# Kernel optimization log

Measured on AMD Instinct MI355X. Metric: run time of the kernel, lower is better.

The kernel has to match this reference:

```python
import jax, jax.numpy as jnp
import numpy as np


def setup_inputs() -> dict:
    key = jax.random.key(0)
    ks = jax.random.split(key, 12)
    C_IN, C = 512, 256  # input_feat_dim, input_feat_dim // 2
    B, H, W = 8, 14, 14
    s = 0.02
    return {
        "im": jax.random.normal(ks[0], (B, C_IN, H, W), dtype=jnp.float32),
        "boxes": jax.random.normal(ks[1], (B, 4, 4), dtype=jnp.float32),
        "normalized_boxes": jax.random.normal(ks[2], (B, 4, 4), dtype=jnp.float32),
        # proj: Conv2d(512, 256, kernel_size=1) -> equivalent to [out, in] matmul
        "proj_w": jax.random.normal(ks[3], (C, C_IN), dtype=jnp.float32) * s,
        "proj_b": jax.random.normal(ks[4], (C,), dtype=jnp.float32) * s,
        # g_mlp: Linear(512,256), Linear(256,256), Linear(256,256); stored [in, out]
        "w1": jax.random.normal(ks[5], (2 * C, C), dtype=jnp.float32) * s,
        "b1": jax.random.normal(ks[6], (C,), dtype=jnp.float32) * s,
        "w2": jax.random.normal(ks[7], (C, C), dtype=jnp.float32) * s,
        "b2": jax.random.normal(ks[8], (C,), dtype=jnp.float32) * s,
        "w3": jax.random.normal(ks[9], (C, C), dtype=jnp.float32) * s,
        "b3": jax.random.normal(ks[10], (C,), dtype=jnp.float32) * s,
    }


def reference(im, boxes, normalized_boxes, proj_w, proj_b, w1, b1, w2, b2, w3, b3):
    # boxes / normalized_boxes are deleted by the original forward.
    del boxes, normalized_boxes
    # 1x1 conv projection: [b, c_in, h, w] -> [b, c, h, w]
    x = jnp.einsum("bihw,oi->bohw", im, proj_w) + proj_b[None, :, None, None]
    b, c, h, w = x.shape
    hw = h * w
    xf = x.reshape(b, c, hw).transpose(0, 2, 1)  # [b, hw, c]
    # Pairwise concat semantics of the original:
    #   x_full[b, k, l, :] = concat(x_flat[b, l], x_flat[b, k])
    # First Linear on the concat decomposes: xf @ w1[:c] indexed by l,
    # xf @ w1[c:] indexed by k (same math, avoids materializing the 2c concat).
    a_l = xf @ w1[:c]   # [b, hw, c] -> broadcast over k
    a_k = xf @ w1[c:]   # [b, hw, c] -> broadcast over l
    h1 = jax.nn.relu(a_k[:, :, None, :] + a_l[:, None, :, :] + b1)  # [b, hw, hw, c]
    h2 = jax.nn.relu(h1 @ w2 + b2)
    h3 = jax.nn.relu(h2 @ w3 + b3)  # Dropout(0.5) is identity at inference
    # sum over all hw*hw pairs -> [b, c]
    return h3.sum(axis=(1, 2))
```

## Files before the change

### kernel.cpp

```cpp
#include <hip/hip_runtime.h>
#include <hip/hip_bf16.h>

typedef unsigned short u16;
typedef float  f32x4  __attribute__((ext_vector_type(4)));
typedef __bf16 bf16x8 __attribute__((ext_vector_type(8)));
typedef unsigned short u16x8 __attribute__((ext_vector_type(8)));
typedef unsigned short u16x4 __attribute__((ext_vector_type(4)));

__device__ __forceinline__ u16 f2bfu(float f) {
    __hip_bfloat16 h = __float2bfloat16(f);
    return __builtin_bit_cast(unsigned short, h);
}

constexpr int kHW = 196;
constexpr int kKC = 25;
constexpr int kLC = 25;
constexpr int kChunks = kKC * kLC;

__global__ __launch_bounds__(256)
void k_prep(const float* __restrict__ pw, u16* __restrict__ pwi,
            const float* __restrict__ w1, u16* __restrict__ w1li, u16* __restrict__ w1ki,
            const float* __restrict__ w2, u16* __restrict__ w2i,
            const float* __restrict__ w3, u16* __restrict__ w3i) {
    int id = blockIdx.x;
    int n = threadIdx.x;
    if (id < 512) {
        int k = id;
        int kk = k >> 5, kg = (k >> 3) & 3, k8 = k & 7;
        pwi[(((((kk << 2) + kg) << 8) + n) << 3) + k8] = f2bfu(pw[n * 512 + k]);
    } else {
        int k = (id - 512) & 255;
        int kk = k >> 5, kg = (k >> 3) & 3, k8 = k & 7;
        int idx = (((((kk << 2) + kg) << 8) + n) << 3) + k8;
        if (id < 768)       w1li[idx] = f2bfu(w1[k * 256 + n]);
        else if (id < 1024) w1ki[idx] = f2bfu(w1[(k + 256) * 256 + n]);
        else if (id < 1280) w2i[idx]  = f2bfu(w2[k * 256 + n]);
        else                w3i[idx]  = f2bfu(w3[k * 256 + n]);
    }
}

__global__ __launch_bounds__(256, 2)
void k_xa3(const float* __restrict__ im, const u16* __restrict__ pwi,
           const float* __restrict__ pb, const u16* __restrict__ w1li,
           const u16* __restrict__ w1ki, float* __restrict__ al,
           float* __restrict__ ak) {
    __shared__ u16 imT[16 * 512];
    __shared__ u16 xfs[16 * 256];
    const int tid = threadIdx.x;
    const int b = blockIdx.y;
    const int p0 = blockIdx.x * 14;

    {
        int t4 = tid & 3;
        int ibase = tid >> 2;
#pragma unroll
        for (int it = 0; it < 8; ++it) {
            int i = it * 64 + ibase;
            const float* src = im + (b * 512 + i) * kHW;
#pragma unroll
            for (int j = 0; j < 4; ++j) {
                int prow = t4 * 4 + j;
                int p = p0 + prow; if (p > 195) p = 195;
                int byte = (prow << 10) + (i << 1);
                byte ^= (prow & 7) << 4;
                *(u16*)((char*)imT + byte) = f2bfu(src[p]);
            }
        }
    }
    __syncthreads();

    const int lane = tid & 63;
    const int wn = tid >> 6;
    const int l15 = lane & 15;
    const int kg = lane >> 4;
    const int wbase = (wn * 64 + l15) << 3;

    f32x4 acc[4];
#pragma unroll
    for (int fn = 0; fn < 4; ++fn) acc[fn] = f32x4{0.f, 0.f, 0.f, 0.f};
    for (int kk = 0; kk < 16; ++kk) {
        int kb = kk * 32 + kg * 8;
        int byte = (l15 << 10) + (kb << 1);
        byte ^= (l15 & 7) << 4;
        bf16x8 hb = __builtin_bit_cast(bf16x8, *(const u16x8*)((const char*)imT + byte));
        const u16* wp = pwi + ((((kk << 2) + kg) << 11) + wbase);
#pragma unroll
        for (int fn = 0; fn < 4; ++fn) {
            bf16x8 aw = __builtin_bit_cast(bf16x8, *(const u16x8*)(wp + (fn << 7)));
            acc[fn] = __builtin_amdgcn_mfma_f32_16x16x32_bf16(aw, hb, acc[fn], 0, 0, 0);
        }
    }
#pragma unroll
    for (int fn = 0; fn < 4; ++fn) {
        f32x4 pbv = *(const f32x4*)(pb + wn * 64 + fn * 16 + kg * 4);
        u16x4 pv;
#pragma unroll
        for (int r = 0; r < 4; ++r) pv[r] = f2bfu(acc[fn][r] + pbv[r]);
        int byte = (l15 << 9) + ((wn * 64 + fn * 16 + kg * 4) << 1);
        byte ^= (l15 & 7) << 4;
        *(u16x4*)((char*)xfs + byte) = pv;
    }
    __syncthreads();

    const int p = p0 + l15;
    const bool valid = (l15 < 14) && (p < kHW);
#pragma unroll
    for (int sel = 0; sel < 2; ++sel) {
        const u16* wsrc = sel ? w1ki : w1li;
        f32x4 a2[4];
#pragma unroll
        for (int fn = 0; fn < 4; ++fn) a2[fn] = f32x4{0.f, 0.f, 0.f, 0.f};
        for (int kk = 0; kk < 8; ++kk) {
            int kb = kk * 32 + kg * 8;
            int byte = (l15 << 9) + (kb << 1);
            byte ^= (l15 & 7) << 4;
            bf16x8 hb = __builtin_bit_cast(bf16x8, *(const u16x8*)((const char*)xfs + byte));
            const u16* wp = wsrc + ((((kk << 2) + kg) << 11) + wbase);
#pragma unroll
            for (int fn = 0; fn < 4; ++fn) {
                bf16x8 aw = __builtin_bit_cast(bf16x8, *(const u16x8*)(wp + (fn << 7)));
                a2[fn] = __builtin_amdgcn_mfma_f32_16x16x32_bf16(aw, hb, a2[fn], 0, 0, 0);
            }
        }
        if (valid) {
            float* dst = (sel ? ak : al) + ((b * kHW + p) << 8) + wn * 64 + kg * 4;
#pragma unroll
            for (int fn = 0; fn < 4; ++fn) *(f32x4*)(dst + fn * 16) = a2[fn];
        }
    }
}

__global__ __launch_bounds__(256, 3)
void k_main7(const float* __restrict__ ak, const float* __restrict__ al,
             const float* __restrict__ b1, const u16* __restrict__ w2i,
             const float* __restrict__ b2, const u16* __restrict__ w3i,
             const float* __restrict__ b3, float* __restrict__ part) {
    __shared__ u16 smem[64 * 256];
    __shared__ float raw[16 * 256];
    const int tid = threadIdx.x;
    const int lc = blockIdx.x, kc = blockIdx.y, b = blockIdx.z;
    const int k0 = kc * 8, l0 = lc * 8;

    {
        int r = tid >> 4;
        int t = tid & 15;
        int src_row = (r < 8) ? (k0 + r) : (l0 + (r - 8));
        if (src_row > 195) src_row = 195;
        const float* src = ((r < 8) ? ak : al) + ((b * kHW + src_row) << 8);
#pragma unroll
        for (int j = 0; j < 4; ++j)
            *(f32x4*)&raw[r * 256 + j * 64 + t * 4] = *(const f32x4*)(src + j * 64 + t * 4);
    }
    __syncthreads();

    {
        const int cc = tid & 31;
        f32x4 c0v = *(const f32x4*)(b1 + (cc << 3));
        f32x4 c1v = *(const f32x4*)(b1 + (cc << 3) + 4);
#pragma unroll
        for (int it = 0; it < 8; ++it) {
            int row = (it * 256 + tid) >> 5;
            const float* akp = &raw[(row >> 3) * 256 + (cc << 3)];
            const float* alp = &raw[(8 + (row & 7)) * 256 + (cc << 3)];
            f32x4 k0v = *(const f32x4*)akp;
            f32x4 k1v = *(const f32x4*)(akp + 4);
            f32x4 l0v = *(const f32x4*)alp;
            f32x4 l1v = *(const f32x4*)(alp + 4);
            u16x8 v;
#pragma unroll
            for (int j = 0; j < 4; ++j) {
                v[j]     = f2bfu(fmaxf(k0v[j] + l0v[j] + c0v[j], 0.f));
                v[4 + j] = f2bfu(fmaxf(k1v[j] + l1v[j] + c1v[j], 0.f));
            }
            int byte = (row << 9) + (cc << 4);
            byte ^= (row & 7) << 4;
            *(u16x8*)((char*)smem + byte) = v;
        }
    }
    __syncthreads();

    const int lane = tid & 63;
    const int wn = tid >> 6;
    const int l15 = lane & 15;
    const int kg = lane >> 4;

    f32x4 acc[4][4];
    const int wbase = (wn * 64 + l15) << 3;

#pragma unroll
    for (int fn = 0; fn < 4; ++fn)
#pragma unroll
        for (int fm = 0; fm < 4; ++fm) acc[fn][fm] = f32x4{0.f, 0.f, 0.f, 0.f};
    for (int kk = 0; kk < 8; ++kk) {
        int kb = kk * 32 + kg * 8;
        bf16x8 hb[4];
#pragma unroll
        for (int fm = 0; fm < 4; ++fm) {
            int row = fm * 16 + l15;
            int byte = (row << 9) + (kb << 1);
            byte ^= (row & 7) << 4;
            hb[fm] = __builtin_bit_cast(bf16x8, *(const u16x8*)((const char*)smem + byte));
        }
        const u16* wp = w2i + ((((kk << 2) + kg) << 11) + wbase);
#pragma unroll
        for (int fn = 0; fn < 4; ++fn) {
            bf16x8 aw = __builtin_bit_cast(bf16x8, *(const u16x8*)(wp + (fn << 7)));
#pragma unroll
            for (int fm = 0; fm < 4; ++fm)
                acc[fn][fm] = __builtin_amdgcn_mfma_f32_16x16x32_bf16(aw, hb[fm], acc[fn][fm], 0, 0, 0);
        }
    }
    __syncthreads();

#pragma unroll
    for (int fn = 0; fn < 4; ++fn) {
        f32x4 b2v = *(const f32x4*)(b2 + wn * 64 + fn * 16 + kg * 4);
#pragma unroll
        for (int fm = 0; fm < 4; ++fm) {
            int prow = fm * 16 + l15;
            u16x4 pv;
#pragma unroll
            for (int r = 0; r < 4; ++r)
                pv[r] = f2bfu(fmaxf(acc[fn][fm][r] + b2v[r], 0.f));
            int byte = (prow << 9) + ((wn * 64 + fn * 16 + kg * 4) << 1);
            byte ^= (prow & 7) << 4;
            *(u16x4*)((char*)smem + byte) = pv;
        }
    }
    __syncthreads();

#pragma unroll
    for (int fn = 0; fn < 4; ++fn)
#pragma unroll
        for (int fm = 0; fm < 4; ++fm) acc[fn][fm] = f32x4{0.f, 0.f, 0.f, 0.f};
    for (int kk = 0; kk < 8; ++kk) {
        int kb = kk * 32 + kg * 8;
        bf16x8 hb[4];
#pragma unroll
        for (int fm = 0; fm < 4; ++fm) {
            int row = fm * 16 + l15;
            int byte = (row << 9) + (kb << 1);
            byte ^= (row & 7) << 4;
            hb[fm] = __builtin_bit_cast(bf16x8, *(const u16x8*)((const char*)smem + byte));
        }
        const u16* wp = w3i + ((((kk << 2) + kg) << 11) + wbase);
#pragma unroll
        for (int fn = 0; fn < 4; ++fn) {
            bf16x8 aw = __builtin_bit_cast(bf16x8, *(const u16x8*)(wp + (fn << 7)));
#pragma unroll
            for (int fm = 0; fm < 4; ++fm)
                acc[fn][fm] = __builtin_amdgcn_mfma_f32_16x16x32_bf16(aw, hb[fm], acc[fn][fm], 0, 0, 0);
        }
    }

    float s[4][4] = {};
#pragma unroll
    for (int fm = 0; fm < 4; ++fm) {
        int pr = fm * 16 + l15;
        int ki = k0 + (pr >> 3);
        int li = l0 + (pr & 7);
        float vm = (ki < kHW && li < kHW) ? 1.f : 0.f;
#pragma unroll
        for (int fn = 0; fn < 4; ++fn) {
            f32x4 b3v = *(const f32x4*)(b3 + wn * 64 + fn * 16 + kg * 4);
#pragma unroll
            for (int r = 0; r < 4; ++r)
                s[fn][r] += vm * fmaxf(acc[fn][fm][r] + b3v[r], 0.f);
        }
    }
#pragma unroll
    for (int fn = 0; fn < 4; ++fn)
#pragma unroll
        for (int r = 0; r < 4; ++r) {
            s[fn][r] += __shfl_xor(s[fn][r], 1);
            s[fn][r] += __shfl_xor(s[fn][r], 2);
            s[fn][r] += __shfl_xor(s[fn][r], 4);
            s[fn][r] += __shfl_xor(s[fn][r], 8);
        }
    if (l15 == 0) {
        int chunkid = (b * kKC + kc) * kLC + lc;
        float* pp = part + chunkid * 256 + wn * 64 + kg * 4;
#pragma unroll
        for (int fn = 0; fn < 4; ++fn)
            *(f32x4*)(pp + fn * 16) = f32x4{s[fn][0], s[fn][1], s[fn][2], s[fn][3]};
    }
}

__global__ __launch_bounds__(1024)
void k_reduce(const float* __restrict__ part, float* __restrict__ out) {
    __shared__ float red[4][256];
    int b = blockIdx.x;
    int c = threadIdx.x & 255;
    int stripe = threadIdx.x >> 8;
    const float* p = part + (b * kChunks) * 256 + c;
    float s = 0.f;
    for (int j = stripe; j < kChunks; j += 4) s += p[j * 256];
    red[stripe][c] = s;
    __syncthreads();
    if (threadIdx.x < 256)
        out[b * 256 + threadIdx.x] = red[0][threadIdx.x] + red[1][threadIdx.x] +
                                     red[2][threadIdx.x] + red[3][threadIdx.x];
}

extern "C" void kernel_launch(void* const* d_in, const int* in_sizes, int n_in,
                              void* d_out, int out_size, void* d_ws, size_t ws_size,
                              hipStream_t stream) {
    const float* im = (const float*)d_in[0];
    const float* pw = (const float*)d_in[3];
    const float* pb = (const float*)d_in[4];
    const float* w1 = (const float*)d_in[5];
    const float* b1 = (const float*)d_in[6];
    const float* w2 = (const float*)d_in[7];
    const float* b2 = (const float*)d_in[8];
    const float* w3 = (const float*)d_in[9];
    const float* b3 = (const float*)d_in[10];
    float* out = (float*)d_out;

    float* al  = (float*)d_ws;
    float* ak  = al + 8 * 196 * 256;
    u16* pwi  = (u16*)(ak + 8 * 196 * 256);
    u16* w1li = pwi + 512 * 256;
    u16* w1ki = w1li + 256 * 256;
    u16* w2i  = w1ki + 256 * 256;
    u16* w3i  = w2i + 256 * 256;
    float* part = (float*)(w3i + 256 * 256);

    hipLaunchKernelGGL(k_prep, dim3(1536), dim3(256), 0, stream,
                       pw, pwi, w1, w1li, w1ki, w2, w2i, w3, w3i);
    hipLaunchKernelGGL(k_xa3, dim3(14, 8), dim3(256), 0, stream,
                       im, pwi, pb, w1li, w1ki, al, ak);
    hipLaunchKernelGGL(k_main7, dim3(kLC, kKC, 8), dim3(256), 0, stream,
                       ak, al, b1, w2i, b2, w3i, b3, part);
    hipLaunchKernelGGL(k_reduce, dim3(8), dim3(1024), 0, stream, part, out);
}
```

Before: 151.7 us.

## Switch pair MLP to 32x32x16 MFMA and fuse reduction via atomics

The two 256x256 matmuls in the main kernel now use 32x32x16 bf16 MFMA tiles instead of 16x16x32, with a wider LDS swizzle and raised wave priority around the MFMA loops. The per-chunk partial buffer and the separate reduce kernel are removed. Each block instead atomically adds its channel sums into the output, which the prep kernel zeroes. This cuts one launch and the partial-sum traffic, and the larger MFMA shape should raise matrix throughput. The cost is atomic contention on the output and a nondeterministic summation order.

```diff
diff --git a/kernel.cpp b/kernel.cpp
--- a/kernel.cpp
+++ b/kernel.cpp
@@ -3,6 +3,7 @@
 
 typedef unsigned short u16;
 typedef float  f32x4  __attribute__((ext_vector_type(4)));
+typedef float  f32x16 __attribute__((ext_vector_type(16)));
 typedef __bf16 bf16x8 __attribute__((ext_vector_type(8)));
 typedef unsigned short u16x8 __attribute__((ext_vector_type(8)));
 typedef unsigned short u16x4 __attribute__((ext_vector_type(4)));
@@ -15,27 +16,27 @@
 constexpr int kHW = 196;
 constexpr int kKC = 25;
 constexpr int kLC = 25;
-constexpr int kChunks = kKC * kLC;
 
 __global__ __launch_bounds__(256)
 void k_prep(const float* __restrict__ pw, u16* __restrict__ pwi,
             const float* __restrict__ w1, u16* __restrict__ w1li, u16* __restrict__ w1ki,
             const float* __restrict__ w2, u16* __restrict__ w2i,
-            const float* __restrict__ w3, u16* __restrict__ w3i) {
+            const float* __restrict__ w3, u16* __restrict__ w3i,
+            float* __restrict__ out) {
     int id = blockIdx.x;
     int n = threadIdx.x;
     if (id < 512) {
         int k = id;
-        int kk = k >> 5, kg = (k >> 3) & 3, k8 = k & 7;
-        pwi[(((((kk << 2) + kg) << 8) + n) << 3) + k8] = f2bfu(pw[n * 512 + k]);
-    } else {
+        pwi[((k >> 3) << 11) + (n << 3) + (k & 7)] = f2bfu(pw[n * 512 + k]);
+    } else if (id < 1536) {
         int k = (id - 512) & 255;
-        int kk = k >> 5, kg = (k >> 3) & 3, k8 = k & 7;
-        int idx = (((((kk << 2) + kg) << 8) + n) << 3) + k8;
+        int idx = ((k >> 3) << 11) + (n << 3) + (k & 7);
         if (id < 768)       w1li[idx] = f2bfu(w1[k * 256 + n]);
         else if (id < 1024) w1ki[idx] = f2bfu(w1[(k + 256) * 256 + n]);
         else if (id < 1280) w2i[idx]  = f2bfu(w2[k * 256 + n]);
         else                w3i[idx]  = f2bfu(w3[k * 256 + n]);
+    } else {
+        out[(id - 1536) * 256 + n] = 0.f;
     }
 }
 
@@ -131,10 +132,10 @@
 }
 
 __global__ __launch_bounds__(256, 3)
-void k_main7(const float* __restrict__ ak, const float* __restrict__ al,
+void k_main8(const float* __restrict__ ak, const float* __restrict__ al,
              const float* __restrict__ b1, const u16* __restrict__ w2i,
              const float* __restrict__ b2, const u16* __restrict__ w3i,
-             const float* __restrict__ b3, float* __restrict__ part) {
+             const float* __restrict__ b3, float* __restrict__ out) {
     __shared__ u16 smem[64 * 256];
     __shared__ float raw[16 * 256];
     const int tid = threadIdx.x;
@@ -142,8 +143,7 @@
     const int k0 = kc * 8, l0 = lc * 8;
 
     {
-        int r = tid >> 4;
-        int t = tid & 15;
+        int r = tid >> 4, t = tid & 15;
         int src_row = (r < 8) ? (k0 + r) : (l0 + (r - 8));
         if (src_row > 195) src_row = 195;
         const float* src = ((r < 8) ? ak : al) + ((b * kHW + src_row) << 8);
@@ -173,7 +173,7 @@
                 v[4 + j] = f2bfu(fmaxf(k1v[j] + l1v[j] + c1v[j], 0.f));
             }
             int byte = (row << 9) + (cc << 4);
-            byte ^= (row & 7) << 4;
+            byte ^= (row & 15) << 4;
             *(u16x8*)((char*)smem + byte) = v;
         }
     }
@@ -181,125 +181,128 @@
 
     const int lane = tid & 63;
     const int wn = tid >> 6;
-    const int l15 = lane & 15;
-    const int kg = lane >> 4;
-
-    f32x4 acc[4][4];
-    const int wbase = (wn * 64 + l15) << 3;
-
-#pragma unroll
-    for (int fn = 0; fn < 4; ++fn)
-#pragma unroll
-        for (int fm = 0; fm < 4; ++fm) acc[fn][fm] = f32x4{0.f, 0.f, 0.f, 0.f};
-    for (int kk = 0; kk < 8; ++kk) {
-        int kb = kk * 32 + kg * 8;
-        bf16x8 hb[4];
-#pragma unroll
-        for (int fm = 0; fm < 4; ++fm) {
-            int row = fm * 16 + l15;
-            int byte = (row << 9) + (kb << 1);
-            byte ^= (row & 7) << 4;
-            hb[fm] = __builtin_bit_cast(bf16x8, *(const u16x8*)((const char*)smem + byte));
-        }
-        const u16* wp = w2i + ((((kk << 2) + kg) << 11) + wbase);
-#pragma unroll
-        for (int fn = 0; fn < 4; ++fn) {
-            bf16x8 aw = __builtin_bit_cast(bf16x8, *(const u16x8*)(wp + (fn << 7)));
-#pragma unroll
-            for (int fm = 0; fm < 4; ++fm)
-                acc[fn][fm] = __builtin_amdgcn_mfma_f32_16x16x32_bf16(aw, hb[fm], acc[fn][fm], 0, 0, 0);
-        }
-    }
-    __syncthreads();
-
-#pragma unroll
-    for (int fn = 0; fn < 4; ++fn) {
-        f32x4 b2v = *(const f32x4*)(b2 + wn * 64 + fn * 16 + kg * 4);
-#pragma unroll
-        for (int fm = 0; fm < 4; ++fm) {
-            int prow = fm * 16 + l15;
-            u16x4 pv;
-#pragma unroll
-            for (int r = 0; r < 4; ++r)
-                pv[r] = f2bfu(fmaxf(acc[fn][fm][r] + b2v[r], 0.f));
-            int byte = (prow << 9) + ((wn * 64 + fn * 16 + kg * 4) << 1);
-            byte ^= (prow & 7) << 4;
-            *(u16x4*)((char*)smem + byte) = pv;
-        }
-    }
-    __syncthreads();
-
-#pragma unroll
-    for (int fn = 0; fn < 4; ++fn)
-#pragma unroll
-        for (int fm = 0; fm < 4; ++fm) acc[fn][fm] = f32x4{0.f, 0.f, 0.f, 0.f};
-    for (int kk = 0; kk < 8; ++kk) {
-        int kb = kk * 32 + kg * 8;
-        bf16x8 hb[4];
-#pragma unroll
-        for (int fm = 0; fm < 4; ++fm) {
-            int row = fm * 16 + l15;
-            int byte = (row << 9) + (kb << 1);
-            byte ^= (row & 7) << 4;
-            hb[fm] = __builtin_bit_cast(bf16x8, *(const u16x8*)((const char*)smem + byte));
-        }
-        const u16* wp = w3i + ((((kk << 2) + kg) << 11) + wbase);
-#pragma unroll
-        for (int fn = 0; fn < 4; ++fn) {
-            bf16x8 aw = __builtin_bit_cast(bf16x8, *(const u16x8*)(wp + (fn << 7)));
-#pragma unroll
-            for (int fm = 0; fm < 4; ++fm)
-                acc[fn][fm] = __builtin_amdgcn_mfma_f32_16x16x32_bf16(aw, hb[fm], acc[fn][fm], 0, 0, 0);
-        }
-    }
-
-    float s[4][4] = {};
-#pragma unroll
-    for (int fm = 0; fm < 4; ++fm) {
-        int pr = fm * 16 + l15;
-        int ki = k0 + (pr >> 3);
-        int li = l0 + (pr & 7);
-        float vm = (ki < kHW && li < kHW) ? 1.f : 0.f;
-#pragma unroll
-        for (int fn = 0; fn < 4; ++fn) {
-            f32x4 b3v = *(const f32x4*)(b3 + wn * 64 + fn * 16 + kg * 4);
-#pragma unroll
-            for (int r = 0; r < 4; ++r)
-                s[fn][r] += vm * fmaxf(acc[fn][fm][r] + b3v[r], 0.f);
-        }
-    }
-#pragma unroll
-    for (int fn = 0; fn < 4; ++fn)
-#pragma unroll
-        for (int r = 0; r < 4; ++r) {
-            s[fn][r] += __shfl_xor(s[fn][r], 1);
-            s[fn][r] += __shfl_xor(s[fn][r], 2);
-            s[fn][r] += __shfl_xor(s[fn][r], 4);
-            s[fn][r] += __shfl_xor(s[fn][r], 8);
-        }
-    if (l15 == 0) {
-        int chunkid = (b * kKC + kc) * kLC + lc;
-        float* pp = part + chunkid * 256 + wn * 64 + kg * 4;
-#pragma unroll
-        for (int fn = 0; fn < 4; ++fn)
-            *(f32x4*)(pp + fn * 16) = f32x4{s[fn][0], s[fn][1], s[fn][2], s[fn][3]};
-    }
-}
-
-__global__ __launch_bounds__(1024)
-void k_reduce(const float* __restrict__ part, float* __restrict__ out) {
-    __shared__ float red[4][256];
-    int b = blockIdx.x;
-    int c = threadIdx.x & 255;
-    int stripe = threadIdx.x >> 8;
-    const float* p = part + (b * kChunks) * 256 + c;
-    float s = 0.f;
-    for (int j = stripe; j < kChunks; j += 4) s += p[j * 256];
-    red[stripe][c] = s;
-    __syncthreads();
-    if (threadIdx.x < 256)
-        out[b * 256 + threadIdx.x] = red[0][threadIdx.x] + red[1][threadIdx.x] +
-                                     red[2][threadIdx.x] + red[3][threadIdx.x];
+    const int l31 = lane & 31;
+    const int hi = lane >> 5;
+    const int wbase = (wn * 64 + l31) << 3;
+
+    f32x16 acc[2][2];
+
+#pragma unroll
+    for (int a = 0; a < 2; ++a)
+#pragma unroll
+        for (int c = 0; c < 2; ++c)
+#pragma unroll
+            for (int r = 0; r < 16; ++r) acc[a][c][r] = 0.f;
+    __builtin_amdgcn_s_setprio(1);
+    for (int kk = 0; kk < 16; ++kk) {
+        int kbyte = kk * 32 + hi * 16;
+        bf16x8 hb[2];
+#pragma unroll
+        for (int b32 = 0; b32 < 2; ++b32) {
+            int prow = b32 * 32 + l31;
+            int byte = (prow << 9) + kbyte;
+            byte ^= (prow & 15) << 4;
+            hb[b32] = __builtin_bit_cast(bf16x8, *(const u16x8*)((const char*)smem + byte));
+        }
+        const u16* wp = w2i + (((kk << 1) + hi) << 11) + wbase;
+#pragma unroll
+        for (int a32 = 0; a32 < 2; ++a32) {
+            bf16x8 aw = __builtin_bit_cast(bf16x8, *(const u16x8*)(wp + (a32 << 8)));
+#pragma unroll
+            for (int b32 = 0; b32 < 2; ++b32)
+                acc[a32][b32] = __builtin_amdgcn_mfma_f32_32x32x16_bf16(
+                    aw, hb[b32], acc[a32][b32], 0, 0, 0);
+        }
+    }
+    __builtin_amdgcn_s_setprio(0);
+    __syncthreads();
+
+#pragma unroll
+    for (int a32 = 0; a32 < 2; ++a32) {
+#pragma unroll
+        for (int g = 0; g < 4; ++g) {
+            int ch = wn * 64 + a32 * 32 + hi * 4 + g * 8;
+            f32x4 b2v = *(const f32x4*)(b2 + ch);
+#pragma unroll
+            for (int b32 = 0; b32 < 2; ++b32) {
+                int pair = b32 * 32 + l31;
+                u16x4 pv;
+#pragma unroll
+                for (int m = 0; m < 4; ++m)
+                    pv[m] = f2bfu(fmaxf(acc[a32][b32][g * 4 + m] + b2v[m], 0.f));
+                int byte = (pair << 9) + (ch << 1);
+                byte ^= (pair & 15) << 4;
+                *(u16x4*)((char*)smem + byte) = pv;
+            }
+        }
+    }
+    __syncthreads();
+
+#pragma unroll
+    for (int a = 0; a < 2; ++a)
+#pragma unroll
+        for (int c = 0; c < 2; ++c)
+#pragma unroll
+            for (int r = 0; r < 16; ++r) acc[a][c][r] = 0.f;
+    __builtin_amdgcn_s_setprio(1);
+    for (int kk = 0; kk < 16; ++kk) {
+        int kbyte = kk * 32 + hi * 16;
+        bf16x8 hb[2];
+#pragma unroll
+        for (int b32 = 0; b32 < 2; ++b32) {
+            int prow = b32 * 32 + l31;
+            int byte = (prow << 9) + kbyte;
+            byte ^= (prow & 15) << 4;
+            hb[b32] = __builtin_bit_cast(bf16x8, *(const u16x8*)((const char*)smem + byte));
+        }
+        const u16* wp = w3i + (((kk << 1) + hi) << 11) + wbase;
+#pragma unroll
+        for (int a32 = 0; a32 < 2; ++a32) {
+            bf16x8 aw = __builtin_bit_cast(bf16x8, *(const u16x8*)(wp + (a32 << 8)));
+#pragma unroll
+            for (int b32 = 0; b32 < 2; ++b32)
+                acc[a32][b32] = __builtin_amdgcn_mfma_f32_32x32x16_bf16(
+                    aw, hb[b32], acc[a32][b32], 0, 0, 0);
+        }
+    }
+    __builtin_amdgcn_s_setprio(0);
+
+#pragma unroll
+    for (int a32 = 0; a32 < 2; ++a32) {
+        float s[4][4] = {};
+#pragma unroll
+        for (int b32 = 0; b32 < 2; ++b32) {
+            int pr = b32 * 32 + l31;
+            int ki = k0 + (pr >> 3);
+            int li = l0 + (pr & 7);
+            float vm = (ki < kHW && li < kHW) ? 1.f : 0.f;
+#pragma unroll
+            for (int g = 0; g < 4; ++g) {
+                f32x4 b3v = *(const f32x4*)(b3 + wn * 64 + a32 * 32 + hi * 4 + g * 8);
+#pragma unroll
+                for (int m = 0; m < 4; ++m)
+                    s[g][m] += vm * fmaxf(acc[a32][b32][g * 4 + m] + b3v[m], 0.f);
+            }
+        }
+#pragma unroll
+        for (int g = 0; g < 4; ++g)
+#pragma unroll
+            for (int m = 0; m < 4; ++m) {
+                s[g][m] += __shfl_xor(s[g][m], 1);
+                s[g][m] += __shfl_xor(s[g][m], 2);
+                s[g][m] += __shfl_xor(s[g][m], 4);
+                s[g][m] += __shfl_xor(s[g][m], 8);
+                s[g][m] += __shfl_xor(s[g][m], 16);
+            }
+        if (l31 == 0) {
+            float* op = out + (b << 8) + wn * 64 + a32 * 32 + hi * 4;
+#pragma unroll
+            for (int g = 0; g < 4; ++g)
+#pragma unroll
+                for (int m = 0; m < 4; ++m)
+                    atomicAdd(op + g * 8 + m, s[g][m]);
+        }
+    }
 }
 
 extern "C" void kernel_launch(void* const* d_in, const int* in_sizes, int n_in,
@@ -323,13 +326,11 @@
     u16* w1ki = w1li + 256 * 256;
     u16* w2i  = w1ki + 256 * 256;
     u16* w3i  = w2i + 256 * 256;
-    float* part = (float*)(w3i + 256 * 256);
-
-    hipLaunchKernelGGL(k_prep, dim3(1536), dim3(256), 0, stream,
-                       pw, pwi, w1, w1li, w1ki, w2, w2i, w3, w3i);
+
+    hipLaunchKernelGGL(k_prep, dim3(1544), dim3(256), 0, stream,
+                       pw, pwi, w1, w1li, w1ki, w2, w2i, w3, w3i, out);
     hipLaunchKernelGGL(k_xa3, dim3(14, 8), dim3(256), 0, stream,
                        im, pwi, pb, w1li, w1ki, al, ak);
-    hipLaunchKernelGGL(k_main7, dim3(kLC, kKC, 8), dim3(256), 0, stream,
-                       ak, al, b1, w2i, b2, w3i, b3, part);
-    hipLaunchKernelGGL(k_reduce, dim3(8), dim3(1024), 0, stream, part, out);
-}
+    hipLaunchKernelGGL(k_main8, dim3(kLC, kKC, 8), dim3(256), 0, stream,
+                       ak, al, b1, w2i, b2, w3i, b3, out);
+}
```

Measured after the change: 343.3 us. 126% more time.
